# Kernel optimization log

Measured on AMD Instinct MI355X. Metric: run time of the kernel, lower is better.

The kernel has to match this reference:

```python
import jax, jax.numpy as jnp
import numpy as np

KERNEL = 5
OUT_CAPS = 8
OUT_ATOMS = 32
ROUTINGS = 3


def _squash(x):
    # squash nonlinearity: (|v|^2 / (1+|v|^2)) * v/|v|, over last (atom) axis
    norm = jnp.linalg.norm(x, axis=-1, keepdims=True)
    norm_sq = norm * norm
    return (x / norm) * (norm_sq / (1.0 + norm_sq))


def setup_inputs() -> dict:
    key = jax.random.key(0)
    k1, k2, k3 = jax.random.split(key, 3)
    B, H, Wd, inC, inA = 16, 32, 32, 8, 16
    inputs = jax.random.normal(k1, (B, H, Wd, inC, inA), dtype=jnp.float32)
    # He-normal-ish conv kernel [k, k, inA, outC*outA]
    fan_in = KERNEL * KERNEL * inA
    W = jax.random.normal(k2, (KERNEL, KERNEL, inA, OUT_CAPS * OUT_ATOMS), dtype=jnp.float32) * np.sqrt(2.0 / fan_in)
    b = jnp.full((1, 1, OUT_CAPS, OUT_ATOMS), 0.1, dtype=jnp.float32)
    return {"inputs": inputs, "W": W, "b": b}


def reference(inputs, W, b):
    B, H, Wd, inC, inA = inputs.shape
    # transpose to [inC, B, H, W, inA] and fold capsules into batch for shared conv
    x = jnp.transpose(inputs, (3, 0, 1, 2, 4)).reshape(inC * B, H, Wd, inA)
    conv = jax.lax.conv_general_dilated(
        x, W, window_strides=(1, 1), padding="SAME",
        dimension_numbers=("NHWC", "HWIO", "NHWC"))
    Hp, Wp = conv.shape[1], conv.shape[2]
    # faithful to original TF reshape (row-major) of [inC*B,...] -> [B, inC, ...]
    votes = conv.reshape(B, inC, Hp, Wp, OUT_CAPS, OUT_ATOMS)
    biases = jnp.broadcast_to(b, (Hp, Wp, OUT_CAPS, OUT_ATOMS))

    logits = jnp.zeros((B, inC, Hp, Wp, OUT_CAPS), dtype=votes.dtype)
    act = None
    for _ in range(ROUTINGS):
        route = jax.nn.softmax(logits, axis=-1)  # over output capsules
        # weighted sum of votes over input capsules: [B, Hp, Wp, outC, outA]
        preact = jnp.einsum("bihwc,bihwca->bhwca", route, votes) + biases
        act = _squash(preact)
        # agreement: dot(votes, activation) over atoms -> logit update
        logits = logits + jnp.sum(votes * act[:, None], axis=-1)
    return act
```

## Files before the change

### kernel.cpp

```cpp
#include <hip/hip_runtime.h>


typedef __attribute__((ext_vector_type(2))) _Float16 f16x2;
typedef __attribute__((ext_vector_type(8))) _Float16 f16x8;
typedef __attribute__((ext_vector_type(16))) float f32x16;

union f16x8u { f16x8 v; f16x2 d[4]; unsigned short s[8]; unsigned int u32[4]; unsigned long long u[2]; };
union f16x2u { f16x2 v; unsigned int u; unsigned short s[2]; };

__device__ __forceinline__ unsigned short f2h(float x) {
  union { _Float16 h; unsigned short u; } v;
  v.h = (_Float16)x;
  return v.u;
}

__global__ __launch_bounds__(256) void wprep_kernel(
    const float* __restrict__ W, unsigned short* __restrict__ wsh) {
  int t = blockIdx.x * 256 + threadIdx.x;
  int khkw = t >> 12;
  int rem  = t & 4095;
  int ch = rem >> 4, ia = rem & 15;
  wsh[t] = f2h(W[khkw * 4096 + ia * 256 + ch]);
}

__global__ __launch_bounds__(256, 2) void capsconv_mfma_kernel(
    const float* __restrict__ inp,
    const unsigned short* __restrict__ wsh,
    const float* __restrict__ bias,
    float* __restrict__ out)
{
  __shared__ char smem[17408];
  const _Float16* wshh = (const _Float16*)wsh;

  const int tid  = threadIdx.x;
  const int wid  = tid >> 6;
  const int lane = tid & 63;
  const int sub  = lane >> 5;
  const int ln31 = lane & 31;

  const int bid = blockIdx.x;
  const int wq = bid & 7;
  const int h  = (bid >> 3) & 31;
  const int bb = bid >> 8;
  const int i_src  = bb >> 1;
  const int b_base = (bb & 1) * 8;

  #pragma unroll
  for (int s = 0; s < 5; ++s) {
    int e = tid + s * 256;
    int kh  = e >> 8;
    int ii  = (e >> 5) & 7;
    int wl  = (e >> 2) & 7;
    int iaq = e & 3;
    int hh = h + kh - 2;
    int wsrc = wq * 4 + wl - 2;
    float4 v = make_float4(0.f, 0.f, 0.f, 0.f);
    if ((unsigned)hh < 32u && (unsigned)wsrc < 32u)
      v = *(const float4*)(inp +
          ((((size_t)(b_base + ii) * 32 + hh) * 32 + wsrc) * 8 + i_src) * 16 + iaq * 4);
    union { _Float16 hx[4]; unsigned long long u; } pkk;
    pkk.hx[0] = (_Float16)v.x; pkk.hx[1] = (_Float16)v.y;
    pkk.hx[2] = (_Float16)v.z; pkk.hx[3] = (_Float16)v.w;
    *(unsigned long long*)(smem + kh * 2176 + ii * 272 + wl * 32 + iaq * 8) = pkk.u;
  }
  __syncthreads();

  f32x16 acc[2];
  #pragma unroll
  for (int nt = 0; nt < 2; ++nt)
    #pragma unroll
    for (int e = 0; e < 16; ++e) acc[nt][e] = 0.f;

  const char* aBase = smem + (ln31 & 7) * 272 + (ln31 >> 3) * 32 + sub * 16;
  const _Float16* bBase = wshh + (wid * 64 + ln31) * 16 + sub * 8;

  #pragma unroll
  for (int kh = 0; kh < 5; ++kh) {
    f16x8 af[5], bf0[5], bf1[5];
    #pragma unroll
    for (int kw = 0; kw < 5; ++kw) {
      af[kw]  = *(const f16x8*)(aBase + kh * 2176 + kw * 32);
      bf0[kw] = *(const f16x8*)(bBase + (size_t)(kh * 5 + kw) * 4096);
      bf1[kw] = *(const f16x8*)(bBase + (size_t)(kh * 5 + kw) * 4096 + 512);
    }
    #pragma unroll
    for (int kw = 0; kw < 5; ++kw) {
      acc[0] = __builtin_amdgcn_mfma_f32_32x32x16_f16(af[kw], bf0[kw], acc[0], 0, 0, 0);
      acc[1] = __builtin_amdgcn_mfma_f32_32x32x16_f16(af[kw], bf1[kw], acc[1], 0, 0, 0);
    }
  }

  unsigned int pk[2][4][2];
  #pragma unroll
  for (int nt = 0; nt < 2; ++nt)
    #pragma unroll
    for (int w = 0; w < 4; ++w) {
      f16x2u lo, hi;
      lo.v = f16x2{(_Float16)acc[nt][w * 4 + 0], (_Float16)acc[nt][w * 4 + 1]};
      hi.v = f16x2{(_Float16)acc[nt][w * 4 + 2], (_Float16)acc[nt][w * 4 + 3]};
      pk[nt][w][0] = lo.u; pk[nt][w][1] = hi.u;
    }
  f16x8 vreg[4];
  #pragma unroll
  for (int w = 0; w < 4; ++w) {
    unsigned int own0 = sub ? pk[1][w][0] : pk[0][w][0];
    unsigned int own1 = sub ? pk[1][w][1] : pk[0][w][1];
    unsigned int snd0 = sub ? pk[0][w][0] : pk[1][w][0];
    unsigned int snd1 = sub ? pk[0][w][1] : pk[1][w][1];
    unsigned int rc0 = (unsigned int)__shfl_xor((int)snd0, 32, 64);
    unsigned int rc1 = (unsigned int)__shfl_xor((int)snd1, 32, 64);
    f16x8u vv;
    vv.u32[0] = sub ? rc0 : own0;
    vv.u32[1] = sub ? rc1 : own1;
    vv.u32[2] = sub ? own0 : rc0;
    vv.u32[3] = sub ? own1 : rc1;
    vreg[w] = vv.v;
  }

  __syncthreads();
  #pragma unroll
  for (int w = 0; w < 4; ++w)
    *(f16x8*)(smem + w * 4352 + (tid >> 2) * 68 + (tid & 3) * 16) = vreg[w];
  __syncthreads();

  const int k = lane & 7;
  float vv[4][8];
  #pragma unroll
  for (int j = 0; j < 4; ++j) {
    f16x8u t8;
    t8.v = *(const f16x8*)(smem + wid * 4352 + lane * 68 + j * 16);
    #pragma unroll
    for (int ii = 0; ii < 8; ++ii) vv[j][ii] = (float)t8.v[ii];
  }
  const float4 bv4 = *(const float4*)(bias + lane * 4);
  const float bvj[4] = {bv4.x, bv4.y, bv4.z, bv4.w};

  float logit_k = 0.f;
  float pre[4], scale = 0.f;

  #pragma unroll
  for (int rt = 0; rt < 3; ++rt) {
    float r[8];
    if (rt == 0) {
      #pragma unroll
      for (int i = 0; i < 8; ++i) r[i] = 0.125f;
    } else {
      float mx = logit_k;
      mx = fmaxf(mx, __shfl_xor(mx, 8, 64));
      mx = fmaxf(mx, __shfl_xor(mx, 16, 64));
      mx = fmaxf(mx, __shfl_xor(mx, 32, 64));
      float e = __expf(logit_k - mx);
      float den = e;
      den += __shfl_xor(den, 8, 64);
      den += __shfl_xor(den, 16, 64);
      den += __shfl_xor(den, 32, 64);
      float route_k = e / den;
      int cbase = lane & 56;
      #pragma unroll
      for (int i = 0; i < 8; ++i) r[i] = __shfl(route_k, cbase | i, 64);
    }
    #pragma unroll
    for (int j = 0; j < 4; ++j) {
      float p = bvj[j];
      #pragma unroll
      for (int ii = 0; ii < 8; ++ii) p = fmaf(r[ii], vv[j][ii], p);
      pre[j] = p;
    }
    float nsq = pre[0] * pre[0] + pre[1] * pre[1] + pre[2] * pre[2] + pre[3] * pre[3];
    nsq += __shfl_xor(nsq, 1, 64);
    nsq += __shfl_xor(nsq, 2, 64);
    nsq += __shfl_xor(nsq, 4, 64);
    scale = sqrtf(nsq) / (1.f + nsq);
    if (rt < 2) {
      float dot8[8];
      #pragma unroll
      for (int ii = 0; ii < 8; ++ii) {
        float d = vv[0][ii] * pre[0];
        d = fmaf(vv[1][ii], pre[1], d);
        d = fmaf(vv[2][ii], pre[2], d);
        d = fmaf(vv[3][ii], pre[3], d);
        d += __shfl_xor(d, 1, 64);
        d += __shfl_xor(d, 2, 64);
        d += __shfl_xor(d, 4, 64);
        dot8[ii] = d;
      }
      bool b0 = (k & 1), b1 = (k & 2), b2 = (k & 4);
      float e0 = b0 ? dot8[1] : dot8[0];
      float e1 = b0 ? dot8[3] : dot8[2];
      float e2 = b0 ? dot8[5] : dot8[4];
      float e3 = b0 ? dot8[7] : dot8[6];
      float f0 = b1 ? e1 : e0;
      float f1 = b1 ? e3 : e2;
      logit_k = fmaf(scale, b2 ? f1 : f0, logit_k);
    }
  }
  const size_t pos = (size_t)((bb * 32 + h) * 32 + wq * 4 + wid);
  float4 o = make_float4(pre[0] * scale, pre[1] * scale, pre[2] * scale, pre[3] * scale);
  *(float4*)(out + pos * 256 + lane * 4) = o;
}

extern "C" void kernel_launch(void* const* d_in, const int* in_sizes, int n_in,
                              void* d_out, int out_size, void* d_ws, size_t ws_size,
                              hipStream_t stream) {
  (void)in_sizes; (void)n_in; (void)ws_size; (void)out_size;
  const float* inp  = (const float*)d_in[0];
  const float* W    = (const float*)d_in[1];
  const float* bv   = (const float*)d_in[2];
  float* out        = (float*)d_out;
  unsigned short* wsh = (unsigned short*)d_ws;

  hipLaunchKernelGGL(wprep_kernel, dim3(400), dim3(256), 0, stream, W, wsh);
  hipLaunchKernelGGL(capsconv_mfma_kernel, dim3(4096), dim3(256), 0, stream,
                     inp, wsh, bv, out);
}
```

Before: 57.91 us.

## Double per-block width tile so each B-fragment load feeds two MFMA M-tiles

Each block now computes 8 output columns instead of 4, halving the grid. The input halo tile in shared memory grows to 12 columns, so per-output halo loading shrinks. Each wave issues two M-tiles per weight fragment, halving global weight fragment traffic per output. In exchange, register pressure (4 accumulators, more fragments, double routing state) and shared memory per block rise, which may reduce occupancy under launch_bounds(256,2).

```diff
diff --git a/kernel.cpp b/kernel.cpp
--- a/kernel.cpp
+++ b/kernel.cpp
@@ -29,7 +29,7 @@
     const float* __restrict__ bias,
     float* __restrict__ out)
 {
-  __shared__ char smem[17408];
+  __shared__ char smem[34816];
   const _Float16* wshh = (const _Float16*)wsh;
 
   const int tid  = threadIdx.x;
@@ -39,21 +39,18 @@
   const int ln31 = lane & 31;
 
   const int bid = blockIdx.x;
-  const int wq = bid & 7;
-  const int h  = (bid >> 3) & 31;
-  const int bb = bid >> 8;
+  const int wq = bid & 3;
+  const int h  = (bid >> 2) & 31;
+  const int bb = bid >> 7;
   const int i_src  = bb >> 1;
   const int b_base = (bb & 1) * 8;
 
-  #pragma unroll
-  for (int s = 0; s < 5; ++s) {
-    int e = tid + s * 256;
-    int kh  = e >> 8;
-    int ii  = (e >> 5) & 7;
-    int wl  = (e >> 2) & 7;
-    int iaq = e & 3;
+  for (int e = tid; e < 1920; e += 256) {
+    int kh = e / 384; int r1 = e - kh * 384;
+    int ii = r1 / 48; int r2 = r1 - ii * 48;
+    int wl = r2 >> 2; int iaq = r2 & 3;
     int hh = h + kh - 2;
-    int wsrc = wq * 4 + wl - 2;
+    int wsrc = wq * 8 + wl - 2;
     float4 v = make_float4(0.f, 0.f, 0.f, 0.f);
     if ((unsigned)hh < 32u && (unsigned)wsrc < 32u)
       v = *(const float4*)(inp +
@@ -61,142 +58,161 @@
     union { _Float16 hx[4]; unsigned long long u; } pkk;
     pkk.hx[0] = (_Float16)v.x; pkk.hx[1] = (_Float16)v.y;
     pkk.hx[2] = (_Float16)v.z; pkk.hx[3] = (_Float16)v.w;
-    *(unsigned long long*)(smem + kh * 2176 + ii * 272 + wl * 32 + iaq * 8) = pkk.u;
+    *(unsigned long long*)(smem + kh * 3200 + ii * 400 + wl * 32 + iaq * 8) = pkk.u;
   }
   __syncthreads();
 
-  f32x16 acc[2];
-  #pragma unroll
-  for (int nt = 0; nt < 2; ++nt)
-    #pragma unroll
-    for (int e = 0; e < 16; ++e) acc[nt][e] = 0.f;
-
-  const char* aBase = smem + (ln31 & 7) * 272 + (ln31 >> 3) * 32 + sub * 16;
+  f32x16 acc[2][2];
+  #pragma unroll
+  for (int mt = 0; mt < 2; ++mt)
+    #pragma unroll
+    for (int nt = 0; nt < 2; ++nt)
+      #pragma unroll
+      for (int e = 0; e < 16; ++e) acc[mt][nt][e] = 0.f;
+
+  const char* aBase = smem + (ln31 & 7) * 400 + (ln31 >> 3) * 32 + sub * 16;
   const _Float16* bBase = wshh + (wid * 64 + ln31) * 16 + sub * 8;
 
   #pragma unroll
   for (int kh = 0; kh < 5; ++kh) {
-    f16x8 af[5], bf0[5], bf1[5];
+    f16x8 af0[5], af1[5], bf0[5], bf1[5];
     #pragma unroll
     for (int kw = 0; kw < 5; ++kw) {
-      af[kw]  = *(const f16x8*)(aBase + kh * 2176 + kw * 32);
+      af0[kw] = *(const f16x8*)(aBase + kh * 3200 + kw * 32);
+      af1[kw] = *(const f16x8*)(aBase + kh * 3200 + (kw + 4) * 32);
       bf0[kw] = *(const f16x8*)(bBase + (size_t)(kh * 5 + kw) * 4096);
       bf1[kw] = *(const f16x8*)(bBase + (size_t)(kh * 5 + kw) * 4096 + 512);
     }
     #pragma unroll
     for (int kw = 0; kw < 5; ++kw) {
-      acc[0] = __builtin_amdgcn_mfma_f32_32x32x16_f16(af[kw], bf0[kw], acc[0], 0, 0, 0);
-      acc[1] = __builtin_amdgcn_mfma_f32_32x32x16_f16(af[kw], bf1[kw], acc[1], 0, 0, 0);
-    }
-  }
-
-  unsigned int pk[2][4][2];
-  #pragma unroll
-  for (int nt = 0; nt < 2; ++nt)
-    #pragma unroll
-    for (int w = 0; w < 4; ++w) {
-      f16x2u lo, hi;
-      lo.v = f16x2{(_Float16)acc[nt][w * 4 + 0], (_Float16)acc[nt][w * 4 + 1]};
-      hi.v = f16x2{(_Float16)acc[nt][w * 4 + 2], (_Float16)acc[nt][w * 4 + 3]};
-      pk[nt][w][0] = lo.u; pk[nt][w][1] = hi.u;
-    }
-  f16x8 vreg[4];
-  #pragma unroll
-  for (int w = 0; w < 4; ++w) {
-    unsigned int own0 = sub ? pk[1][w][0] : pk[0][w][0];
-    unsigned int own1 = sub ? pk[1][w][1] : pk[0][w][1];
-    unsigned int snd0 = sub ? pk[0][w][0] : pk[1][w][0];
-    unsigned int snd1 = sub ? pk[0][w][1] : pk[1][w][1];
-    unsigned int rc0 = (unsigned int)__shfl_xor((int)snd0, 32, 64);
-    unsigned int rc1 = (unsigned int)__shfl_xor((int)snd1, 32, 64);
-    f16x8u vv;
-    vv.u32[0] = sub ? rc0 : own0;
-    vv.u32[1] = sub ? rc1 : own1;
-    vv.u32[2] = sub ? own0 : rc0;
-    vv.u32[3] = sub ? own1 : rc1;
-    vreg[w] = vv.v;
-  }
+      acc[0][0] = __builtin_amdgcn_mfma_f32_32x32x16_f16(af0[kw], bf0[kw], acc[0][0], 0, 0, 0);
+      acc[0][1] = __builtin_amdgcn_mfma_f32_32x32x16_f16(af0[kw], bf1[kw], acc[0][1], 0, 0, 0);
+      acc[1][0] = __builtin_amdgcn_mfma_f32_32x32x16_f16(af1[kw], bf0[kw], acc[1][0], 0, 0, 0);
+      acc[1][1] = __builtin_amdgcn_mfma_f32_32x32x16_f16(af1[kw], bf1[kw], acc[1][1], 0, 0, 0);
+    }
+  }
+
+  unsigned int pk[2][2][4][2];
+  #pragma unroll
+  for (int mt = 0; mt < 2; ++mt)
+    #pragma unroll
+    for (int nt = 0; nt < 2; ++nt)
+      #pragma unroll
+      for (int q = 0; q < 4; ++q) {
+        f16x2u lo, hi;
+        lo.v = f16x2{(_Float16)acc[mt][nt][q * 4 + 0], (_Float16)acc[mt][nt][q * 4 + 1]};
+        hi.v = f16x2{(_Float16)acc[mt][nt][q * 4 + 2], (_Float16)acc[mt][nt][q * 4 + 3]};
+        pk[mt][nt][q][0] = lo.u; pk[mt][nt][q][1] = hi.u;
+      }
+  f16x8 vreg[8];
+  #pragma unroll
+  for (int mt = 0; mt < 2; ++mt)
+    #pragma unroll
+    for (int q = 0; q < 4; ++q) {
+      unsigned int own0 = sub ? pk[mt][1][q][0] : pk[mt][0][q][0];
+      unsigned int own1 = sub ? pk[mt][1][q][1] : pk[mt][0][q][1];
+      unsigned int snd0 = sub ? pk[mt][0][q][0] : pk[mt][1][q][0];
+      unsigned int snd1 = sub ? pk[mt][0][q][1] : pk[mt][1][q][1];
+      unsigned int rc0 = (unsigned int)__shfl_xor((int)snd0, 32, 64);
+      unsigned int rc1 = (unsigned int)__shfl_xor((int)snd1, 32, 64);
+      f16x8u vv;
+      vv.u32[0] = sub ? rc0 : own0;
+      vv.u32[1] = sub ? rc1 : own1;
+      vv.u32[2] = sub ? own0 : rc0;
+      vv.u32[3] = sub ? own1 : rc1;
+      vreg[mt * 4 + q] = vv.v;
+    }
 
   __syncthreads();
   #pragma unroll
-  for (int w = 0; w < 4; ++w)
+  for (int w = 0; w < 8; ++w)
     *(f16x8*)(smem + w * 4352 + (tid >> 2) * 68 + (tid & 3) * 16) = vreg[w];
   __syncthreads();
 
   const int k = lane & 7;
-  float vv[4][8];
-  #pragma unroll
-  for (int j = 0; j < 4; ++j) {
-    f16x8u t8;
-    t8.v = *(const f16x8*)(smem + wid * 4352 + lane * 68 + j * 16);
-    #pragma unroll
-    for (int ii = 0; ii < 8; ++ii) vv[j][ii] = (float)t8.v[ii];
-  }
+  float vv[2][4][8];
+  #pragma unroll
+  for (int p = 0; p < 2; ++p)
+    #pragma unroll
+    for (int j = 0; j < 4; ++j) {
+      f16x8u t8;
+      t8.v = *(const f16x8*)(smem + (wid * 2 + p) * 4352 + lane * 68 + j * 16);
+      #pragma unroll
+      for (int ii = 0; ii < 8; ++ii) vv[p][j][ii] = (float)t8.v[ii];
+    }
   const float4 bv4 = *(const float4*)(bias + lane * 4);
   const float bvj[4] = {bv4.x, bv4.y, bv4.z, bv4.w};
 
-  float logit_k = 0.f;
-  float pre[4], scale = 0.f;
+  float logit_k[2] = {0.f, 0.f};
+  float pre[2][4], scale[2] = {0.f, 0.f};
 
   #pragma unroll
   for (int rt = 0; rt < 3; ++rt) {
-    float r[8];
-    if (rt == 0) {
-      #pragma unroll
-      for (int i = 0; i < 8; ++i) r[i] = 0.125f;
-    } else {
-      float mx = logit_k;
-      mx = fmaxf(mx, __shfl_xor(mx, 8, 64));
-      mx = fmaxf(mx, __shfl_xor(mx, 16, 64));
-      mx = fmaxf(mx, __shfl_xor(mx, 32, 64));
-      float e = __expf(logit_k - mx);
-      float den = e;
-      den += __shfl_xor(den, 8, 64);
-      den += __shfl_xor(den, 16, 64);
-      den += __shfl_xor(den, 32, 64);
-      float route_k = e / den;
-      int cbase = lane & 56;
-      #pragma unroll
-      for (int i = 0; i < 8; ++i) r[i] = __shfl(route_k, cbase | i, 64);
-    }
-    #pragma unroll
-    for (int j = 0; j < 4; ++j) {
-      float p = bvj[j];
-      #pragma unroll
-      for (int ii = 0; ii < 8; ++ii) p = fmaf(r[ii], vv[j][ii], p);
-      pre[j] = p;
-    }
-    float nsq = pre[0] * pre[0] + pre[1] * pre[1] + pre[2] * pre[2] + pre[3] * pre[3];
-    nsq += __shfl_xor(nsq, 1, 64);
-    nsq += __shfl_xor(nsq, 2, 64);
-    nsq += __shfl_xor(nsq, 4, 64);
-    scale = sqrtf(nsq) / (1.f + nsq);
-    if (rt < 2) {
-      float dot8[8];
-      #pragma unroll
-      for (int ii = 0; ii < 8; ++ii) {
-        float d = vv[0][ii] * pre[0];
-        d = fmaf(vv[1][ii], pre[1], d);
-        d = fmaf(vv[2][ii], pre[2], d);
-        d = fmaf(vv[3][ii], pre[3], d);
-        d += __shfl_xor(d, 1, 64);
-        d += __shfl_xor(d, 2, 64);
-        d += __shfl_xor(d, 4, 64);
-        dot8[ii] = d;
-      }
-      bool b0 = (k & 1), b1 = (k & 2), b2 = (k & 4);
-      float e0 = b0 ? dot8[1] : dot8[0];
-      float e1 = b0 ? dot8[3] : dot8[2];
-      float e2 = b0 ? dot8[5] : dot8[4];
-      float e3 = b0 ? dot8[7] : dot8[6];
-      float f0 = b1 ? e1 : e0;
-      float f1 = b1 ? e3 : e2;
-      logit_k = fmaf(scale, b2 ? f1 : f0, logit_k);
-    }
-  }
-  const size_t pos = (size_t)((bb * 32 + h) * 32 + wq * 4 + wid);
-  float4 o = make_float4(pre[0] * scale, pre[1] * scale, pre[2] * scale, pre[3] * scale);
-  *(float4*)(out + pos * 256 + lane * 4) = o;
+    #pragma unroll
+    for (int p = 0; p < 2; ++p) {
+      float r[8];
+      if (rt == 0) {
+        #pragma unroll
+        for (int i = 0; i < 8; ++i) r[i] = 0.125f;
+      } else {
+        float mx = logit_k[p];
+        mx = fmaxf(mx, __shfl_xor(mx, 8, 64));
+        mx = fmaxf(mx, __shfl_xor(mx, 16, 64));
+        mx = fmaxf(mx, __shfl_xor(mx, 32, 64));
+        float e = __expf(logit_k[p] - mx);
+        float den = e;
+        den += __shfl_xor(den, 8, 64);
+        den += __shfl_xor(den, 16, 64);
+        den += __shfl_xor(den, 32, 64);
+        float route_k = e / den;
+        int cbase = lane & 56;
+        #pragma unroll
+        for (int i = 0; i < 8; ++i) r[i] = __shfl(route_k, cbase | i, 64);
+      }
+      #pragma unroll
+      for (int j = 0; j < 4; ++j) {
+        float pp = bvj[j];
+        #pragma unroll
+        for (int ii = 0; ii < 8; ++ii) pp = fmaf(r[ii], vv[p][j][ii], pp);
+        pre[p][j] = pp;
+      }
+      float nsq = pre[p][0] * pre[p][0] + pre[p][1] * pre[p][1] +
+                  pre[p][2] * pre[p][2] + pre[p][3] * pre[p][3];
+      nsq += __shfl_xor(nsq, 1, 64);
+      nsq += __shfl_xor(nsq, 2, 64);
+      nsq += __shfl_xor(nsq, 4, 64);
+      scale[p] = sqrtf(nsq) / (1.f + nsq);
+      if (rt < 2) {
+        float dot8[8];
+        #pragma unroll
+        for (int ii = 0; ii < 8; ++ii) {
+          float d = vv[p][0][ii] * pre[p][0];
+          d = fmaf(vv[p][1][ii], pre[p][1], d);
+          d = fmaf(vv[p][2][ii], pre[p][2], d);
+          d = fmaf(vv[p][3][ii], pre[p][3], d);
+          d += __shfl_xor(d, 1, 64);
+          d += __shfl_xor(d, 2, 64);
+          d += __shfl_xor(d, 4, 64);
+          dot8[ii] = d;
+        }
+        bool b0 = (k & 1), b1 = (k & 2), b2 = (k & 4);
+        float e0 = b0 ? dot8[1] : dot8[0];
+        float e1 = b0 ? dot8[3] : dot8[2];
+        float e2 = b0 ? dot8[5] : dot8[4];
+        float e3 = b0 ? dot8[7] : dot8[6];
+        float f0 = b1 ? e1 : e0;
+        float f1 = b1 ? e3 : e2;
+        logit_k[p] = fmaf(scale[p], b2 ? f1 : f0, logit_k[p]);
+      }
+    }
+  }
+  const size_t base8 = (size_t)((bb * 32 + h) * 32 + wq * 8);
+  #pragma unroll
+  for (int p = 0; p < 2; ++p) {
+    float4 o = make_float4(pre[p][0] * scale[p], pre[p][1] * scale[p],
+                           pre[p][2] * scale[p], pre[p][3] * scale[p]);
+    *(float4*)(out + (base8 + wid * 2 + p) * 256 + lane * 4) = o;
+  }
 }
 
 extern "C" void kernel_launch(void* const* d_in, const int* in_sizes, int n_in,
@@ -210,6 +226,6 @@
   unsigned short* wsh = (unsigned short*)d_ws;
 
   hipLaunchKernelGGL(wprep_kernel, dim3(400), dim3(256), 0, stream, W, wsh);
-  hipLaunchKernelGGL(capsconv_mfma_kernel, dim3(4096), dim3(256), 0, stream,
+  hipLaunchKernelGGL(capsconv_mfma_kernel, dim3(2048), dim3(256), 0, stream,
                      inp, wsh, bv, out);
 }
```

After: 54.88 us. -5.2%, faster.
